# Kernel optimization log

Hardware: AMD Instinct MI355X
Metric: run time of the kernel (lower is better)

## Reference

```python
import jax, jax.numpy as jnp
import numpy as np

N = 100000      # nodes
E = 1600000     # edges (avg degree 16)
H = 128         # hidden channels
L = 5           # num_layers (only valid range 4<num_layers<8 for this module; 4 index-errors)
ALPHA = 0.1
THETA = 0.5
EPS = 1e-5      # BatchNorm1d default eps


def setup_inputs() -> dict:
    key = jax.random.key(0)
    ks = jax.random.split(key, 8)
    x = jax.random.normal(ks[0], (N, H), dtype=jnp.float32)
    W_in = jax.random.normal(ks[1], (H, H), dtype=jnp.float32) / np.float32(np.sqrt(H))
    b_in = jnp.zeros((H,), jnp.float32)
    conv_W = jax.random.normal(ks[2], (L, H, H), dtype=jnp.float32) / np.float32(np.sqrt(H))
    bn_gamma = jnp.ones((L - 1, H), jnp.float32)
    bn_beta = jnp.zeros((L - 1, H), jnp.float32)
    W_jk = jax.random.normal(ks[3], (4 * H, H), dtype=jnp.float32) / np.float32(np.sqrt(4 * H))
    b_jk = jnp.zeros((H,), jnp.float32)
    src = jax.random.randint(ks[4], (E,), 0, N, dtype=jnp.int32).astype(jnp.int64)
    dst = jax.random.randint(ks[5], (E,), 0, N, dtype=jnp.int32).astype(jnp.int64)
    return dict(x=x, W_in=W_in, b_in=b_in, conv_W=conv_W, bn_gamma=bn_gamma,
                bn_beta=bn_beta, W_jk=W_jk, b_jk=b_jk, src=src, dst=dst)


def _batchnorm(z, gamma, beta):
    # BatchNorm1d, training-mode batch statistics over the node dimension
    m = z.mean(axis=0)
    v = z.var(axis=0)
    return (z - m) * jax.lax.rsqrt(v + EPS) * gamma + beta


def reference(x, W_in, b_in, conv_W, bn_gamma, bn_beta, W_jk, b_jk, src, dst):
    # lins[0]
    z = x @ W_in + b_in          # [N, H]
    x0 = z                       # initial residual for GCNII
    zs = []
    for i in range(L):
        # GCN2Conv (shared_weights=True, normalize=False):
        #   msg = A @ z  (sparse propagation over edge list)
        msg = jax.ops.segment_sum(z[src], dst, num_segments=N)   # [N, H]
        h = (1.0 - ALPHA) * msg + ALPHA * x0
        beta_l = float(np.log(THETA / (i + 1) + 1.0))
        z = (1.0 - beta_l) * h + beta_l * (h @ conv_W[i])
        zs.append(z)
        if i % 4 == 3:
            # JumpingKnowledge('cat') over the 4 layer outputs, then lins[-1].
            # (Original code also applies BN here but immediately overwrites z,
            #  so that BN is dead computation and is skipped.)
            z = jnp.concatenate(zs[:4], axis=-1) @ W_jk + b_jk   # [N, H]
        elif i < L - 1:
            z = jax.nn.relu(_batchnorm(z, bn_gamma[i], bn_beta[i]))
    return z
```

## Files before the change

kernel.cpp:

```cpp
#include <hip/hip_runtime.h>
#include <hip/hip_bf16.h>
#include <cmath>
#include <cstddef>

#define NN 100000
#define HH 128
#define EE 1600000
#define NH (NN * HH)
#define ALPHA_C 0.1f
#define THETA_C 0.5f
#define EPS_C 1e-5f

constexpr int TR = 64;
constexpr int AST = 68;
constexpr int SCAN_B = 256;
constexpr int NBLK = (NN + SCAN_B - 1) / SCAN_B;

__global__ __launch_bounds__(256) void zero_int_k(int* __restrict__ p, int n) {
    int i = blockIdx.x * 256 + threadIdx.x;
    if (i < n) p[i] = 0;
}
__global__ __launch_bounds__(256) void zero_f4_k(float4* __restrict__ p, int n4) {
    int i = blockIdx.x * 256 + threadIdx.x;
    if (i < n4) p[i] = float4{0.f, 0.f, 0.f, 0.f};
}

__global__ void detect_idx64(const int* __restrict__ p, int* __restrict__ flag) {
    int any = 0;
    for (int i = 0; i < 64; ++i) any |= p[2 * i + 1];
    *flag = (any == 0) ? 1 : 0;
}

__device__ __forceinline__ int load_idx(const void* p, int e, int is64) {
    return is64 ? (int)((const long long*)p)[e] : ((const int*)p)[e];
}

__global__ __launch_bounds__(256) void hist_k(
    const void* __restrict__ dstp, const int* __restrict__ flag,
    int* __restrict__ hist)
{
    int e = blockIdx.x * 256 + threadIdx.x;
    if (e >= EE) return;
    atomicAdd(&hist[load_idx(dstp, e, *flag)], 1);
}

__global__ __launch_bounds__(SCAN_B) void scan1_k(
    const int* __restrict__ hist, int* __restrict__ incl, int* __restrict__ bsum)
{
    __shared__ int sh[SCAN_B];
    int t = threadIdx.x;
    int i = blockIdx.x * SCAN_B + t;
    int v = (i < NN) ? hist[i] : 0;
    sh[t] = v;
    __syncthreads();
    for (int off = 1; off < SCAN_B; off <<= 1) {
        int x = (t >= off) ? sh[t - off] : 0;
        __syncthreads();
        sh[t] += x;
        __syncthreads();
    }
    if (i < NN) incl[i] = sh[t];
    if (t == SCAN_B - 1) bsum[blockIdx.x] = sh[t];
}

__global__ __launch_bounds__(512) void scan2_k(int* __restrict__ bsum) {
    __shared__ int sh[512];
    int t = threadIdx.x;
    sh[t] = (t < NBLK) ? bsum[t] : 0;
    __syncthreads();
    for (int off = 1; off < 512; off <<= 1) {
        int x = (t >= off) ? sh[t - off] : 0;
        __syncthreads();
        sh[t] += x;
        __syncthreads();
    }
    if (t < NBLK) bsum[t] = sh[t];
}

__global__ __launch_bounds__(SCAN_B) void scan3_k(
    const int* __restrict__ hist, const int* __restrict__ incl,
    const int* __restrict__ bsum, int* __restrict__ row_ptr,
    int* __restrict__ cursor)
{
    int b = blockIdx.x;
    int i = b * SCAN_B + threadIdx.x;
    if (i < NN) {
        int ex = incl[i] - hist[i] + (b > 0 ? bsum[b - 1] : 0);
        row_ptr[i] = ex;
        cursor[i] = ex;
    }
    if (i == 0) row_ptr[NN] = EE;
}

__global__ __launch_bounds__(256) void fill_k(
    const void* __restrict__ srcp, const void* __restrict__ dstp,
    const int* __restrict__ flag, int* __restrict__ cursor,
    int* __restrict__ sorted_src)
{
    int e = blockIdx.x * 256 + threadIdx.x;
    if (e >= EE) return;
    int is64 = *flag;
    int d = load_idx(dstp, e, is64);
    int pos = atomicAdd(&cursor[d], 1);
    sorted_src[pos] = load_idx(srcp, e, is64);
}

__global__ __launch_bounds__(256) void gather_k(
    const float* __restrict__ z, const int* __restrict__ row_ptr,
    const int* __restrict__ sorted_src,
    const float* __restrict__ stats,
    const float* __restrict__ gamma, const float* __restrict__ beta,
    float* __restrict__ msg)
{
    int node = blockIdx.x * 4 + (threadIdx.x >> 6);
    if (node >= NN) return;
    int lane = threadIdx.x & 63;
    int half = lane >> 5;
    int c4 = lane & 31;

    const bool bn = (stats != nullptr);
    float4 sc = {1.f, 1.f, 1.f, 1.f}, sh = {0.f, 0.f, 0.f, 0.f};
    if (bn) {
        const float invN = 1.f / (float)NN;
        float4 s  = ((const float4*)stats)[c4];
        float4 s2 = ((const float4*)(stats + 128))[c4];
        float4 g  = ((const float4*)gamma)[c4];
        float4 b  = ((const float4*)beta)[c4];
        float m, var;
        m = s.x * invN; var = s2.x * invN - m * m;
        sc.x = rsqrtf(var + EPS_C) * g.x; sh.x = b.x - m * sc.x;
        m = s.y * invN; var = s2.y * invN - m * m;
        sc.y = rsqrtf(var + EPS_C) * g.y; sh.y = b.y - m * sc.y;
        m = s.z * invN; var = s2.z * invN - m * m;
        sc.z = rsqrtf(var + EPS_C) * g.z; sh.z = b.z - m * sc.z;
        m = s.w * invN; var = s2.w * invN - m * m;
        sc.w = rsqrtf(var + EPS_C) * g.w; sh.w = b.w - m * sc.w;
    }

    int e0 = row_ptr[node], e1 = row_ptr[node + 1];
    float4 acc = {0.f, 0.f, 0.f, 0.f};
    for (int e = e0 + half; e < e1; e += 2) {
        int s = sorted_src[e];
        float4 v = ((const float4*)(z + (size_t)s * HH))[c4];
        if (bn) {
            v.x = fmaxf(0.f, v.x * sc.x + sh.x);
            v.y = fmaxf(0.f, v.y * sc.y + sh.y);
            v.z = fmaxf(0.f, v.z * sc.z + sh.z);
            v.w = fmaxf(0.f, v.w * sc.w + sh.w);
        }
        acc.x += v.x; acc.y += v.y; acc.z += v.z; acc.w += v.w;
    }
    acc.x += __shfl_down(acc.x, 32);
    acc.y += __shfl_down(acc.y, 32);
    acc.z += __shfl_down(acc.z, 32);
    acc.w += __shfl_down(acc.w, 32);
    if (half == 0)
        ((float4*)(msg + (size_t)node * HH))[c4] = acc;
}

__global__ __launch_bounds__(256) void prep_w(
    const float* __restrict__ W_in, const float* __restrict__ conv_W,
    float* __restrict__ Wp)
{
    int i = blockIdx.y;
    int idx = blockIdx.x * 256 + threadIdx.x;
    float v;
    if (i == 0) {
        v = W_in[idx];
    } else {
        float bl = logf(THETA_C / (float)i + 1.f);
        int k = idx >> 7, c = idx & 127;
        v = bl * conv_W[(size_t)(i - 1) * 16384 + idx] + ((k == c) ? (1.f - bl) : 0.f);
    }
    Wp[(size_t)i * 16384 + idx] = v;
}

__global__ __launch_bounds__(256, 4) void gemm128(
    const float* __restrict__ src0, const float* __restrict__ src1,
    float cA, float cB, const float* __restrict__ Wp,
    const float* __restrict__ bias, float* __restrict__ out,
    float* __restrict__ statsp, int nrows)
{
    __shared__ float As[HH * AST];
    const int t = threadIdx.x;
    const int tx = t & 31;
    const int ty = t >> 5;
    const int lane = t & 63, w = t >> 6;
    const int row0 = blockIdx.x * TR;
    const bool useB = (cB != 0.f);

#pragma unroll
    for (int i = 0; i < 8; ++i) {
        int r = (i & 3) * 16 + (lane & 15);
        int k4 = ((i >> 2) * 4 + w) * 4 + (lane >> 4);
        float4 v = {0.f, 0.f, 0.f, 0.f};
        if (row0 + r < nrows) {
            float4 a = ((const float4*)(src0 + (size_t)(row0 + r) * HH))[k4];
            if (useB) {
                float4 b = ((const float4*)(src1 + (size_t)(row0 + r) * HH))[k4];
                v.x = cA * a.x + cB * b.x; v.y = cA * a.y + cB * b.y;
                v.z = cA * a.z + cB * b.z; v.w = cA * a.w + cB * b.w;
            } else {
                v.x = cA * a.x; v.y = cA * a.y; v.z = cA * a.z; v.w = cA * a.w;
            }
        }
        int k = k4 * 4;
        As[(k + 0) * AST + r] = v.x;
        As[(k + 1) * AST + r] = v.y;
        As[(k + 2) * AST + r] = v.z;
        As[(k + 3) * AST + r] = v.w;
    }
    __syncthreads();

    float acc[8][4];
#pragma unroll
    for (int ii = 0; ii < 8; ++ii)
#pragma unroll
        for (int j = 0; j < 4; ++j) acc[ii][j] = 0.f;

    const float4* W4 = (const float4*)Wp;
    float4 wbuf[4];
#pragma unroll
    for (int kk = 0; kk < 4; ++kk) wbuf[kk] = W4[kk * 32 + tx];

    for (int k0 = 0; k0 < HH; k0 += 4) {
        float4 wn[4];
        const bool more = (k0 + 4 < HH);
#pragma unroll
        for (int kk = 0; kk < 4; ++kk) {
            if (more) wn[kk] = W4[(k0 + 4 + kk) * 32 + tx];
            int k = k0 + kk;
            const float* ap = &As[k * AST + ty * 8];
            float4 a0 = *(const float4*)ap;
            float4 a1 = *(const float4*)(ap + 4);
            float a[8] = {a0.x, a0.y, a0.z, a0.w, a1.x, a1.y, a1.z, a1.w};
#pragma unroll
            for (int ii = 0; ii < 8; ++ii) {
                acc[ii][0] += a[ii] * wbuf[kk].x;
                acc[ii][1] += a[ii] * wbuf[kk].y;
                acc[ii][2] += a[ii] * wbuf[kk].z;
                acc[ii][3] += a[ii] * wbuf[kk].w;
            }
        }
        if (more) {
#pragma unroll
            for (int kk = 0; kk < 4; ++kk) wbuf[kk] = wn[kk];
        }
    }

    float4 b4 = {0.f, 0.f, 0.f, 0.f};
    if (bias) b4 = ((const float4*)bias)[tx];
    float cs[4] = {0.f, 0.f, 0.f, 0.f}, cq[4] = {0.f, 0.f, 0.f, 0.f};
    const bool doStats = (statsp != nullptr);
#pragma unroll
    for (int ii = 0; ii < 8; ++ii) {
        int r = row0 + ty * 8 + ii;
        if (r < nrows) {
            float4 v = {acc[ii][0] + b4.x, acc[ii][1] + b4.y,
                        acc[ii][2] + b4.z, acc[ii][3] + b4.w};
            ((float4*)out)[(size_t)r * 32 + tx] = v;
            if (doStats) {
                cs[0] += v.x; cq[0] += v.x * v.x;
                cs[1] += v.y; cq[1] += v.y * v.y;
                cs[2] += v.z; cq[2] += v.z * v.z;
                cs[3] += v.w; cq[3] += v.w * v.w;
            }
        }
    }
    if (doStats) {
        __syncthreads();
        float* red = As;
#pragma unroll
        for (int j = 0; j < 4; ++j) {
            red[ty * 128 + tx * 4 + j] = cs[j];
            red[1024 + ty * 128 + tx * 4 + j] = cq[j];
        }
        __syncthreads();
        if (t < 128) {
            float s = 0.f, q = 0.f;
#pragma unroll
            for (int g = 0; g < 8; ++g) {
                s += red[g * 128 + t];
                q += red[1024 + g * 128 + t];
            }
            atomicAdd(&statsp[t], s);
            atomicAdd(&statsp[128 + t], q);
        }
    }
}

__global__ __launch_bounds__(256, 4) void gemm_jk(
    const float* __restrict__ z0, const float* __restrict__ z1,
    const float* __restrict__ z2, const float* __restrict__ z3,
    const float* __restrict__ Wjk, const float* __restrict__ bjk,
    float* __restrict__ out, int nrows)
{
    __shared__ float As[HH * AST];
    const int t = threadIdx.x;
    const int tx = t & 31;
    const int ty = t >> 5;
    const int lane = t & 63, w = t >> 6;
    const int row0 = blockIdx.x * TR;

    float acc[8][4];
#pragma unroll
    for (int ii = 0; ii < 8; ++ii)
#pragma unroll
        for (int j = 0; j < 4; ++j) acc[ii][j] = 0.f;

    const float* srcs[4] = {z0, z1, z2, z3};
    for (int j = 0; j < 4; ++j) {
        if (j) __syncthreads();
        const float* Z = srcs[j];
#pragma unroll
        for (int i = 0; i < 8; ++i) {
            int r = (i & 3) * 16 + (lane & 15);
            int k4 = ((i >> 2) * 4 + w) * 4 + (lane >> 4);
            float4 v = {0.f, 0.f, 0.f, 0.f};
            if (row0 + r < nrows)
                v = ((const float4*)(Z + (size_t)(row0 + r) * HH))[k4];
            int k = k4 * 4;
            As[(k + 0) * AST + r] = v.x;
            As[(k + 1) * AST + r] = v.y;
            As[(k + 2) * AST + r] = v.z;
            As[(k + 3) * AST + r] = v.w;
        }
        __syncthreads();

        const float4* W4 = (const float4*)(Wjk + (size_t)j * 128 * HH);
        float4 wbuf[4];
#pragma unroll
        for (int kk = 0; kk < 4; ++kk) wbuf[kk] = W4[kk * 32 + tx];

        for (int k0 = 0; k0 < HH; k0 += 4) {
            float4 wn[4];
            const bool more = (k0 + 4 < HH);
#pragma unroll
            for (int kk = 0; kk < 4; ++kk) {
                if (more) wn[kk] = W4[(k0 + 4 + kk) * 32 + tx];
                int k = k0 + kk;
                const float* ap = &As[k * AST + ty * 8];
                float4 a0 = *(const float4*)ap;
                float4 a1 = *(const float4*)(ap + 4);
                float a[8] = {a0.x, a0.y, a0.z, a0.w, a1.x, a1.y, a1.z, a1.w};
#pragma unroll
                for (int ii = 0; ii < 8; ++ii) {
                    acc[ii][0] += a[ii] * wbuf[kk].x;
                    acc[ii][1] += a[ii] * wbuf[kk].y;
                    acc[ii][2] += a[ii] * wbuf[kk].z;
                    acc[ii][3] += a[ii] * wbuf[kk].w;
                }
            }
            if (more) {
#pragma unroll
                for (int kk = 0; kk < 4; ++kk) wbuf[kk] = wn[kk];
            }
        }
    }

    float4 b4 = ((const float4*)bjk)[tx];
#pragma unroll
    for (int ii = 0; ii < 8; ++ii) {
        int r = row0 + ty * 8 + ii;
        if (r < nrows) {
            float4 v = {acc[ii][0] + b4.x, acc[ii][1] + b4.y,
                        acc[ii][2] + b4.z, acc[ii][3] + b4.w};
            ((float4*)out)[(size_t)r * 32 + tx] = v;
        }
    }
}

extern "C" void kernel_launch(void* const* d_in, const int* in_sizes, int n_in,
                              void* d_out, int out_size, void* d_ws, size_t ws_size,
                              hipStream_t stream)
{
    const float* x       = (const float*)d_in[0];
    const float* W_in    = (const float*)d_in[1];
    const float* b_in    = (const float*)d_in[2];
    const float* conv_W  = (const float*)d_in[3];
    const float* bn_g    = (const float*)d_in[4];
    const float* bn_b    = (const float*)d_in[5];
    const float* W_jk    = (const float*)d_in[6];
    const float* b_jk    = (const float*)d_in[7];
    const void*  srcp    = d_in[8];
    const void*  dstp    = d_in[9];

    float* ws     = (float*)d_ws;
    float* x0     = ws;
    float* msg    = ws + (size_t)NH;
    float* zs0    = ws + 2 * (size_t)NH;
    float* zs1    = ws + 3 * (size_t)NH;
    float* zs2    = ws + 4 * (size_t)NH;
    float* stats3 = ws + 5 * (size_t)NH;
    int*   flag       = (int*)(stats3 + 768);
    int*   hist       = flag + 1;
    int*   incl       = hist + NN;
    int*   row_ptr    = incl + NN;
    int*   cursor     = row_ptr + NN + 1;
    int*   bsum       = cursor + NN;
    int*   sorted_src = bsum + NBLK + 1;
    float* Wp         = (float*)(sorted_src + EE);

    const int GEMM_GRID = (NN + TR - 1) / TR;
    const int EDGE_GRID = (EE + 255) / 256;
    const int NODE_GRID = (NN + 3) / 4;

    detect_idx64<<<1, 1, 0, stream>>>((const int*)srcp, flag);
    zero_int_k<<<(NN + 255) / 256, 256, 0, stream>>>(hist, NN);
    zero_f4_k<<<1, 192, 0, stream>>>((float4*)stats3, 192);
    hist_k<<<EDGE_GRID, 256, 0, stream>>>(dstp, flag, hist);
    scan1_k<<<NBLK, SCAN_B, 0, stream>>>(hist, incl, bsum);
    scan2_k<<<1, 512, 0, stream>>>(bsum);
    scan3_k<<<NBLK, SCAN_B, 0, stream>>>(hist, incl, bsum, row_ptr, cursor);
    fill_k<<<EDGE_GRID, 256, 0, stream>>>(srcp, dstp, flag, cursor, sorted_src);
    prep_w<<<dim3(64, 6), 256, 0, stream>>>(W_in, conv_W, Wp);

    gemm128<<<GEMM_GRID, 256, 0, stream>>>(x, x, 1.f, 0.f, Wp, b_in, x0,
                                           nullptr, NN);

    const float* act = x0;
    const float* stats_cur = nullptr;
    const float* g_cur = nullptr;
    const float* b_cur = nullptr;

    for (int i = 0; i < 5; ++i) {
        gather_k<<<NODE_GRID, 256, 0, stream>>>(act, row_ptr, sorted_src,
                                                stats_cur, g_cur, b_cur, msg);

        float* zraw = (i >= 3) ? (float*)d_out : (zs0 + (size_t)i * NH);
        float* stats_next = (i < 3) ? (stats3 + (size_t)i * 256) : nullptr;
        gemm128<<<GEMM_GRID, 256, 0, stream>>>(msg, x0, 1.f - ALPHA_C, ALPHA_C,
                                               Wp + (size_t)(i + 1) * 16384,
                                               nullptr, zraw, stats_next, NN);
        if (i < 3) {
            act = zraw;
            stats_cur = stats_next;
            g_cur = bn_g + (size_t)i * HH;
            b_cur = bn_b + (size_t)i * HH;
        } else if (i == 3) {
            gemm_jk<<<GEMM_GRID, 256, 0, stream>>>(zs0, zs1, zs2,
                                                   (const float*)d_out, W_jk, b_jk,
                                                   zs0, NN);
            act = zs0;
            stats_cur = nullptr;
            g_cur = nullptr;
            b_cur = nullptr;
        }
    }
}
```

Baseline: 1.603 ms.

## Enlarge GEMM tiles to 128x128 with 8x8 per-thread blocking and swizzled LDS; unroll gather

```diff
diff --git a/kernel.cpp b/kernel.cpp
--- a/kernel.cpp
+++ b/kernel.cpp
@@ -11,8 +11,7 @@
 #define THETA_C 0.5f
 #define EPS_C 1e-5f
 
-constexpr int TR = 64;
-constexpr int AST = 68;
+constexpr int TR = 128;
 constexpr int SCAN_B = 256;
 constexpr int NBLK = (NN + SCAN_B - 1) / SCAN_B;
 
@@ -137,9 +136,29 @@
         sc.w = rsqrtf(var + EPS_C) * g.w; sh.w = b.w - m * sc.w;
     }
 
-    int e0 = row_ptr[node], e1 = row_ptr[node + 1];
+    int e1 = row_ptr[node + 1];
+    int e = row_ptr[node] + half;
     float4 acc = {0.f, 0.f, 0.f, 0.f};
-    for (int e = e0 + half; e < e1; e += 2) {
+    float4 acc2 = {0.f, 0.f, 0.f, 0.f};
+    for (; e + 2 < e1; e += 4) {
+        int s0 = sorted_src[e];
+        int s1 = sorted_src[e + 2];
+        float4 v0 = ((const float4*)(z + (size_t)s0 * HH))[c4];
+        float4 v1 = ((const float4*)(z + (size_t)s1 * HH))[c4];
+        if (bn) {
+            v0.x = fmaxf(0.f, v0.x * sc.x + sh.x);
+            v0.y = fmaxf(0.f, v0.y * sc.y + sh.y);
+            v0.z = fmaxf(0.f, v0.z * sc.z + sh.z);
+            v0.w = fmaxf(0.f, v0.w * sc.w + sh.w);
+            v1.x = fmaxf(0.f, v1.x * sc.x + sh.x);
+            v1.y = fmaxf(0.f, v1.y * sc.y + sh.y);
+            v1.z = fmaxf(0.f, v1.z * sc.z + sh.z);
+            v1.w = fmaxf(0.f, v1.w * sc.w + sh.w);
+        }
+        acc.x += v0.x; acc.y += v0.y; acc.z += v0.z; acc.w += v0.w;
+        acc2.x += v1.x; acc2.y += v1.y; acc2.z += v1.z; acc2.w += v1.w;
+    }
+    if (e < e1) {
         int s = sorted_src[e];
         float4 v = ((const float4*)(z + (size_t)s * HH))[c4];
         if (bn) {
@@ -150,6 +169,7 @@
         }
         acc.x += v.x; acc.y += v.y; acc.z += v.z; acc.w += v.w;
     }
+    acc.x += acc2.x; acc.y += acc2.y; acc.z += acc2.z; acc.w += acc2.w;
     acc.x += __shfl_down(acc.x, 32);
     acc.y += __shfl_down(acc.y, 32);
     acc.z += __shfl_down(acc.z, 32);
@@ -175,24 +195,24 @@
     Wp[(size_t)i * 16384 + idx] = v;
 }
 
-__global__ __launch_bounds__(256, 4) void gemm128(
+__global__ __launch_bounds__(256, 2) void gemm128(
     const float* __restrict__ src0, const float* __restrict__ src1,
     float cA, float cB, const float* __restrict__ Wp,
     const float* __restrict__ bias, float* __restrict__ out,
     float* __restrict__ statsp, int nrows)
 {
-    __shared__ float As[HH * AST];
+    __shared__ float As[HH * 128];
     const int t = threadIdx.x;
-    const int tx = t & 31;
-    const int ty = t >> 5;
+    const int tx = t & 15;
+    const int ty = t >> 4;
     const int lane = t & 63, w = t >> 6;
     const int row0 = blockIdx.x * TR;
     const bool useB = (cB != 0.f);
 
 #pragma unroll
-    for (int i = 0; i < 8; ++i) {
-        int r = (i & 3) * 16 + (lane & 15);
-        int k4 = ((i >> 2) * 4 + w) * 4 + (lane >> 4);
+    for (int i = 0; i < 16; ++i) {
+        int r = (i & 7) * 16 + (lane & 15);
+        int k4 = ((i >> 3) * 4 + w) * 4 + (lane >> 4);
         float4 v = {0.f, 0.f, 0.f, 0.f};
         if (row0 + r < nrows) {
             float4 a = ((const float4*)(src0 + (size_t)(row0 + r) * HH))[k4];
@@ -205,65 +225,85 @@
             }
         }
         int k = k4 * 4;
-        As[(k + 0) * AST + r] = v.x;
-        As[(k + 1) * AST + r] = v.y;
-        As[(k + 2) * AST + r] = v.z;
-        As[(k + 3) * AST + r] = v.w;
+        int rs = r ^ ((k4 & 1) << 4);
+        As[(k + 0) * 128 + rs] = v.x;
+        As[(k + 1) * 128 + rs] = v.y;
+        As[(k + 2) * 128 + rs] = v.z;
+        As[(k + 3) * 128 + rs] = v.w;
     }
     __syncthreads();
 
-    float acc[8][4];
+    float acc[8][8];
 #pragma unroll
     for (int ii = 0; ii < 8; ++ii)
 #pragma unroll
-        for (int j = 0; j < 4; ++j) acc[ii][j] = 0.f;
+        for (int j = 0; j < 8; ++j) acc[ii][j] = 0.f;
 
     const float4* W4 = (const float4*)Wp;
-    float4 wbuf[4];
-#pragma unroll
-    for (int kk = 0; kk < 4; ++kk) wbuf[kk] = W4[kk * 32 + tx];
+    float4 wbA[4], wbB[4];
+#pragma unroll
+    for (int kk = 0; kk < 4; ++kk) {
+        wbA[kk] = W4[kk * 32 + tx];
+        wbB[kk] = W4[kk * 32 + 16 + tx];
+    }
+    const int ty8 = ty * 8;
 
     for (int k0 = 0; k0 < HH; k0 += 4) {
-        float4 wn[4];
+        float4 wnA[4], wnB[4];
         const bool more = (k0 + 4 < HH);
+        const int abase = ty8 ^ (((k0 >> 2) & 1) << 4);
 #pragma unroll
         for (int kk = 0; kk < 4; ++kk) {
-            if (more) wn[kk] = W4[(k0 + 4 + kk) * 32 + tx];
-            int k = k0 + kk;
-            const float* ap = &As[k * AST + ty * 8];
+            if (more) {
+                wnA[kk] = W4[(k0 + 4 + kk) * 32 + tx];
+                wnB[kk] = W4[(k0 + 4 + kk) * 32 + 16 + tx];
+            }
+            const float* ap = &As[(k0 + kk) * 128 + abase];
             float4 a0 = *(const float4*)ap;
             float4 a1 = *(const float4*)(ap + 4);
             float a[8] = {a0.x, a0.y, a0.z, a0.w, a1.x, a1.y, a1.z, a1.w};
+            float4 wA = wbA[kk], wB = wbB[kk];
 #pragma unroll
             for (int ii = 0; ii < 8; ++ii) {
-                acc[ii][0] += a[ii] * wbuf[kk].x;
-                acc[ii][1] += a[ii] * wbuf[kk].y;
-                acc[ii][2] += a[ii] * wbuf[kk].z;
-                acc[ii][3] += a[ii] * wbuf[kk].w;
+                acc[ii][0] += a[ii] * wA.x; acc[ii][1] += a[ii] * wA.y;
+                acc[ii][2] += a[ii] * wA.z; acc[ii][3] += a[ii] * wA.w;
+                acc[ii][4] += a[ii] * wB.x; acc[ii][5] += a[ii] * wB.y;
+                acc[ii][6] += a[ii] * wB.z; acc[ii][7] += a[ii] * wB.w;
             }
         }
         if (more) {
 #pragma unroll
-            for (int kk = 0; kk < 4; ++kk) wbuf[kk] = wn[kk];
-        }
-    }
-
-    float4 b4 = {0.f, 0.f, 0.f, 0.f};
-    if (bias) b4 = ((const float4*)bias)[tx];
-    float cs[4] = {0.f, 0.f, 0.f, 0.f}, cq[4] = {0.f, 0.f, 0.f, 0.f};
+            for (int kk = 0; kk < 4; ++kk) { wbA[kk] = wnA[kk]; wbB[kk] = wnB[kk]; }
+        }
+    }
+
+    float4 bA = {0.f, 0.f, 0.f, 0.f}, bB = {0.f, 0.f, 0.f, 0.f};
+    if (bias) {
+        bA = ((const float4*)bias)[tx];
+        bB = ((const float4*)bias)[16 + tx];
+    }
+    float cs[8] = {0.f, 0.f, 0.f, 0.f, 0.f, 0.f, 0.f, 0.f};
+    float cq[8] = {0.f, 0.f, 0.f, 0.f, 0.f, 0.f, 0.f, 0.f};
     const bool doStats = (statsp != nullptr);
 #pragma unroll
     for (int ii = 0; ii < 8; ++ii) {
-        int r = row0 + ty * 8 + ii;
+        int r = row0 + ty8 + ii;
         if (r < nrows) {
-            float4 v = {acc[ii][0] + b4.x, acc[ii][1] + b4.y,
-                        acc[ii][2] + b4.z, acc[ii][3] + b4.w};
-            ((float4*)out)[(size_t)r * 32 + tx] = v;
+            float4 vA = {acc[ii][0] + bA.x, acc[ii][1] + bA.y,
+                         acc[ii][2] + bA.z, acc[ii][3] + bA.w};
+            float4 vB = {acc[ii][4] + bB.x, acc[ii][5] + bB.y,
+                         acc[ii][6] + bB.z, acc[ii][7] + bB.w};
+            ((float4*)out)[(size_t)r * 32 + tx] = vA;
+            ((float4*)out)[(size_t)r * 32 + 16 + tx] = vB;
             if (doStats) {
-                cs[0] += v.x; cq[0] += v.x * v.x;
-                cs[1] += v.y; cq[1] += v.y * v.y;
-                cs[2] += v.z; cq[2] += v.z * v.z;
-                cs[3] += v.w; cq[3] += v.w * v.w;
+                cs[0] += vA.x; cq[0] += vA.x * vA.x;
+                cs[1] += vA.y; cq[1] += vA.y * vA.y;
+                cs[2] += vA.z; cq[2] += vA.z * vA.z;
+                cs[3] += vA.w; cq[3] += vA.w * vA.w;
+                cs[4] += vB.x; cq[4] += vB.x * vB.x;
+                cs[5] += vB.y; cq[5] += vB.y * vB.y;
+                cs[6] += vB.z; cq[6] += vB.z * vB.z;
+                cs[7] += vB.w; cq[7] += vB.w * vB.w;
             }
         }
     }
@@ -273,15 +313,17 @@
 #pragma unroll
         for (int j = 0; j < 4; ++j) {
             red[ty * 128 + tx * 4 + j] = cs[j];
-            red[1024 + ty * 128 + tx * 4 + j] = cq[j];
+            red[ty * 128 + 64 + tx * 4 + j] = cs[4 + j];
+            red[2048 + ty * 128 + tx * 4 + j] = cq[j];
+            red[2048 + ty * 128 + 64 + tx * 4 + j] = cq[4 + j];
         }
         __syncthreads();
         if (t < 128) {
             float s = 0.f, q = 0.f;
 #pragma unroll
-            for (int g = 0; g < 8; ++g) {
+            for (int g = 0; g < 16; ++g) {
                 s += red[g * 128 + t];
-                q += red[1024 + g * 128 + t];
+                q += red[2048 + g * 128 + t];
             }
             atomicAdd(&statsp[t], s);
             atomicAdd(&statsp[128 + t], q);
@@ -289,83 +331,97 @@
     }
 }
 
-__global__ __launch_bounds__(256, 4) void gemm_jk(
+__global__ __launch_bounds__(256, 2) void gemm_jk(
     const float* __restrict__ z0, const float* __restrict__ z1,
     const float* __restrict__ z2, const float* __restrict__ z3,
     const float* __restrict__ Wjk, const float* __restrict__ bjk,
     float* __restrict__ out, int nrows)
 {
-    __shared__ float As[HH * AST];
+    __shared__ float As[HH * 128];
     const int t = threadIdx.x;
-    const int tx = t & 31;
-    const int ty = t >> 5;
+    const int tx = t & 15;
+    const int ty = t >> 4;
     const int lane = t & 63, w = t >> 6;
     const int row0 = blockIdx.x * TR;
-
-    float acc[8][4];
+    const int ty8 = ty * 8;
+
+    float acc[8][8];
 #pragma unroll
     for (int ii = 0; ii < 8; ++ii)
 #pragma unroll
-        for (int j = 0; j < 4; ++j) acc[ii][j] = 0.f;
+        for (int j = 0; j < 8; ++j) acc[ii][j] = 0.f;
 
     const float* srcs[4] = {z0, z1, z2, z3};
+#pragma unroll
     for (int j = 0; j < 4; ++j) {
         if (j) __syncthreads();
         const float* Z = srcs[j];
 #pragma unroll
-        for (int i = 0; i < 8; ++i) {
-            int r = (i & 3) * 16 + (lane & 15);
-            int k4 = ((i >> 2) * 4 + w) * 4 + (lane >> 4);
+        for (int i = 0; i < 16; ++i) {
+            int r = (i & 7) * 16 + (lane & 15);
+            int k4 = ((i >> 3) * 4 + w) * 4 + (lane >> 4);
             float4 v = {0.f, 0.f, 0.f, 0.f};
             if (row0 + r < nrows)
                 v = ((const float4*)(Z + (size_t)(row0 + r) * HH))[k4];
             int k = k4 * 4;
-            As[(k + 0) * AST + r] = v.x;
-            As[(k + 1) * AST + r] = v.y;
-            As[(k + 2) * AST + r] = v.z;
-            As[(k + 3) * AST + r] = v.w;
+            int rs = r ^ ((k4 & 1) << 4);
+            As[(k + 0) * 128 + rs] = v.x;
+            As[(k + 1) * 128 + rs] = v.y;
+            As[(k + 2) * 128 + rs] = v.z;
+            As[(k + 3) * 128 + rs] = v.w;
         }
         __syncthreads();
 
         const float4* W4 = (const float4*)(Wjk + (size_t)j * 128 * HH);
-        float4 wbuf[4];
-#pragma unroll
-        for (int kk = 0; kk < 4; ++kk) wbuf[kk] = W4[kk * 32 + tx];
+        float4 wbA[4], wbB[4];
+#pragma unroll
+        for (int kk = 0; kk < 4; ++kk) {
+            wbA[kk] = W4[kk * 32 + tx];
+            wbB[kk] = W4[kk * 32 + 16 + tx];
+        }
 
         for (int k0 = 0; k0 < HH; k0 += 4) {
-            float4 wn[4];
+            float4 wnA[4], wnB[4];
             const bool more = (k0 + 4 < HH);
+            const int abase = ty8 ^ (((k0 >> 2) & 1) << 4);
 #pragma unroll
             for (int kk = 0; kk < 4; ++kk) {
-                if (more) wn[kk] = W4[(k0 + 4 + kk) * 32 + tx];
-                int k = k0 + kk;
-                const float* ap = &As[k * AST + ty * 8];
+                if (more) {
+                    wnA[kk] = W4[(k0 + 4 + kk) * 32 + tx];
+                    wnB[kk] = W4[(k0 + 4 + kk) * 32 + 16 + tx];
+                }
+                const float* ap = &As[(k0 + kk) * 128 + abase];
                 float4 a0 = *(const float4*)ap;
                 float4 a1 = *(const float4*)(ap + 4);
                 float a[8] = {a0.x, a0.y, a0.z, a0.w, a1.x, a1.y, a1.z, a1.w};
+                float4 wA = wbA[kk], wB = wbB[kk];
 #pragma unroll
                 for (int ii = 0; ii < 8; ++ii) {
-                    acc[ii][0] += a[ii] * wbuf[kk].x;
-                    acc[ii][1] += a[ii] * wbuf[kk].y;
-                    acc[ii][2] += a[ii] * wbuf[kk].z;
-                    acc[ii][3] += a[ii] * wbuf[kk].w;
+                    acc[ii][0] += a[ii] * wA.x; acc[ii][1] += a[ii] * wA.y;
+                    acc[ii][2] += a[ii] * wA.z; acc[ii][3] += a[ii] * wA.w;
+                    acc[ii][4] += a[ii] * wB.x; acc[ii][5] += a[ii] * wB.y;
+                    acc[ii][6] += a[ii] * wB.z; acc[ii][7] += a[ii] * wB.w;
                 }
             }
             if (more) {
 #pragma unroll
-                for (int kk = 0; kk < 4; ++kk) wbuf[kk] = wn[kk];
-            }
-        }
-    }
-
-    float4 b4 = ((const float4*)bjk)[tx];
+                for (int kk = 0; kk < 4; ++kk) { wbA[kk] = wnA[kk]; wbB[kk] = wnB[kk]; }
+            }
+        }
+    }
+
+    float4 bA = ((const float4*)bjk)[tx];
+    float4 bB = ((const float4*)bjk)[16 + tx];
 #pragma unroll
     for (int ii = 0; ii < 8; ++ii) {
-        int r = row0 + ty * 8 + ii;
+        int r = row0 + ty8 + ii;
         if (r < nrows) {
-            float4 v = {acc[ii][0] + b4.x, acc[ii][1] + b4.y,
-                        acc[ii][2] + b4.z, acc[ii][3] + b4.w};
-            ((float4*)out)[(size_t)r * 32 + tx] = v;
+            float4 vA = {acc[ii][0] + bA.x, acc[ii][1] + bA.y,
+                         acc[ii][2] + bA.z, acc[ii][3] + bA.w};
+            float4 vB = {acc[ii][4] + bB.x, acc[ii][5] + bB.y,
+                         acc[ii][6] + bB.z, acc[ii][7] + bB.w};
+            ((float4*)out)[(size_t)r * 32 + tx] = vA;
+            ((float4*)out)[(size_t)r * 32 + 16 + tx] = vB;
         }
     }
 }
```

New measurement: 1.680 ms. 4.8% more time.

## Fuse residual mix into gather, load GEMM A directly from global, unroll gather

Applied to the files above, without the earlier changes.

```diff
diff --git a/kernel.cpp b/kernel.cpp
--- a/kernel.cpp
+++ b/kernel.cpp
@@ -11,10 +11,11 @@
 #define THETA_C 0.5f
 #define EPS_C 1e-5f
 
-constexpr int TR = 64;
-constexpr int AST = 68;
+constexpr int TRG = 64;
 constexpr int SCAN_B = 256;
 constexpr int NBLK = (NN + SCAN_B - 1) / SCAN_B;
+
+#define AK(v, kk) ((kk) == 0 ? (v).x : (kk) == 1 ? (v).y : (kk) == 2 ? (v).z : (v).w)
 
 __global__ __launch_bounds__(256) void zero_int_k(int* __restrict__ p, int n) {
     int i = blockIdx.x * 256 + threadIdx.x;
@@ -110,6 +111,7 @@
     const int* __restrict__ sorted_src,
     const float* __restrict__ stats,
     const float* __restrict__ gamma, const float* __restrict__ beta,
+    const float* __restrict__ resid,
     float* __restrict__ msg)
 {
     int node = blockIdx.x * 4 + (threadIdx.x >> 6);
@@ -117,6 +119,8 @@
     int lane = threadIdx.x & 63;
     int half = lane >> 5;
     int c4 = lane & 31;
+
+    float4 r4 = ((const float4*)(resid + (size_t)node * HH))[c4];
 
     const bool bn = (stats != nullptr);
     float4 sc = {1.f, 1.f, 1.f, 1.f}, sh = {0.f, 0.f, 0.f, 0.f};
@@ -137,9 +141,29 @@
         sc.w = rsqrtf(var + EPS_C) * g.w; sh.w = b.w - m * sc.w;
     }
 
-    int e0 = row_ptr[node], e1 = row_ptr[node + 1];
+    int e1 = row_ptr[node + 1];
+    int e = row_ptr[node] + half;
     float4 acc = {0.f, 0.f, 0.f, 0.f};
-    for (int e = e0 + half; e < e1; e += 2) {
+    float4 acc2 = {0.f, 0.f, 0.f, 0.f};
+    for (; e + 2 < e1; e += 4) {
+        int s0 = sorted_src[e];
+        int s1 = sorted_src[e + 2];
+        float4 v0 = ((const float4*)(z + (size_t)s0 * HH))[c4];
+        float4 v1 = ((const float4*)(z + (size_t)s1 * HH))[c4];
+        if (bn) {
+            v0.x = fmaxf(0.f, v0.x * sc.x + sh.x);
+            v0.y = fmaxf(0.f, v0.y * sc.y + sh.y);
+            v0.z = fmaxf(0.f, v0.z * sc.z + sh.z);
+            v0.w = fmaxf(0.f, v0.w * sc.w + sh.w);
+            v1.x = fmaxf(0.f, v1.x * sc.x + sh.x);
+            v1.y = fmaxf(0.f, v1.y * sc.y + sh.y);
+            v1.z = fmaxf(0.f, v1.z * sc.z + sh.z);
+            v1.w = fmaxf(0.f, v1.w * sc.w + sh.w);
+        }
+        acc.x += v0.x; acc.y += v0.y; acc.z += v0.z; acc.w += v0.w;
+        acc2.x += v1.x; acc2.y += v1.y; acc2.z += v1.z; acc2.w += v1.w;
+    }
+    if (e < e1) {
         int s = sorted_src[e];
         float4 v = ((const float4*)(z + (size_t)s * HH))[c4];
         if (bn) {
@@ -150,12 +174,17 @@
         }
         acc.x += v.x; acc.y += v.y; acc.z += v.z; acc.w += v.w;
     }
+    acc.x += acc2.x; acc.y += acc2.y; acc.z += acc2.z; acc.w += acc2.w;
     acc.x += __shfl_down(acc.x, 32);
     acc.y += __shfl_down(acc.y, 32);
     acc.z += __shfl_down(acc.z, 32);
     acc.w += __shfl_down(acc.w, 32);
-    if (half == 0)
-        ((float4*)(msg + (size_t)node * HH))[c4] = acc;
+    if (half == 0) {
+        const float cA = 1.f - ALPHA_C, cB = ALPHA_C;
+        float4 o = {cA * acc.x + cB * r4.x, cA * acc.y + cB * r4.y,
+                    cA * acc.z + cB * r4.z, cA * acc.w + cB * r4.w};
+        ((float4*)(msg + (size_t)node * HH))[c4] = o;
+    }
 }
 
 __global__ __launch_bounds__(256) void prep_w(
@@ -175,42 +204,19 @@
     Wp[(size_t)i * 16384 + idx] = v;
 }
 
-__global__ __launch_bounds__(256, 4) void gemm128(
-    const float* __restrict__ src0, const float* __restrict__ src1,
-    float cA, float cB, const float* __restrict__ Wp,
+__global__ __launch_bounds__(256, 3) void gemm128(
+    const float* __restrict__ A, const float* __restrict__ Wp,
     const float* __restrict__ bias, float* __restrict__ out,
     float* __restrict__ statsp, int nrows)
 {
-    __shared__ float As[HH * AST];
+    __shared__ float red[2048];
     const int t = threadIdx.x;
     const int tx = t & 31;
     const int ty = t >> 5;
-    const int lane = t & 63, w = t >> 6;
-    const int row0 = blockIdx.x * TR;
-    const bool useB = (cB != 0.f);
-
-#pragma unroll
-    for (int i = 0; i < 8; ++i) {
-        int r = (i & 3) * 16 + (lane & 15);
-        int k4 = ((i >> 2) * 4 + w) * 4 + (lane >> 4);
-        float4 v = {0.f, 0.f, 0.f, 0.f};
-        if (row0 + r < nrows) {
-            float4 a = ((const float4*)(src0 + (size_t)(row0 + r) * HH))[k4];
-            if (useB) {
-                float4 b = ((const float4*)(src1 + (size_t)(row0 + r) * HH))[k4];
-                v.x = cA * a.x + cB * b.x; v.y = cA * a.y + cB * b.y;
-                v.z = cA * a.z + cB * b.z; v.w = cA * a.w + cB * b.w;
-            } else {
-                v.x = cA * a.x; v.y = cA * a.y; v.z = cA * a.z; v.w = cA * a.w;
-            }
-        }
-        int k = k4 * 4;
-        As[(k + 0) * AST + r] = v.x;
-        As[(k + 1) * AST + r] = v.y;
-        As[(k + 2) * AST + r] = v.z;
-        As[(k + 3) * AST + r] = v.w;
-    }
-    __syncthreads();
+    const int row0o = blockIdx.x * TRG;
+    const int row0 = (row0o <= nrows - TRG) ? row0o : (nrows - TRG);
+    const float4* Ab = (const float4*)(A + (size_t)(row0 + ty * 8) * HH);
+    const float4* W4 = (const float4*)Wp;
 
     float acc[8][4];
 #pragma unroll
@@ -218,33 +224,37 @@
 #pragma unroll
         for (int j = 0; j < 4; ++j) acc[ii][j] = 0.f;
 
-    const float4* W4 = (const float4*)Wp;
-    float4 wbuf[4];
-#pragma unroll
-    for (int kk = 0; kk < 4; ++kk) wbuf[kk] = W4[kk * 32 + tx];
+    float4 ac[8], wc[4];
+#pragma unroll
+    for (int ii = 0; ii < 8; ++ii) ac[ii] = Ab[ii * 32];
+#pragma unroll
+    for (int kk = 0; kk < 4; ++kk) wc[kk] = W4[kk * 32 + tx];
 
     for (int k0 = 0; k0 < HH; k0 += 4) {
-        float4 wn[4];
         const bool more = (k0 + 4 < HH);
+        const int c4n = (k0 >> 2) + 1;
+        float4 an[8], wn[4];
+        if (more) {
+#pragma unroll
+            for (int kk = 0; kk < 4; ++kk) wn[kk] = W4[(k0 + 4 + kk) * 32 + tx];
+#pragma unroll
+            for (int ii = 0; ii < 8; ++ii) an[ii] = Ab[ii * 32 + c4n];
+        }
 #pragma unroll
         for (int kk = 0; kk < 4; ++kk) {
-            if (more) wn[kk] = W4[(k0 + 4 + kk) * 32 + tx];
-            int k = k0 + kk;
-            const float* ap = &As[k * AST + ty * 8];
-            float4 a0 = *(const float4*)ap;
-            float4 a1 = *(const float4*)(ap + 4);
-            float a[8] = {a0.x, a0.y, a0.z, a0.w, a1.x, a1.y, a1.z, a1.w};
+            float4 w = wc[kk];
 #pragma unroll
             for (int ii = 0; ii < 8; ++ii) {
-                acc[ii][0] += a[ii] * wbuf[kk].x;
-                acc[ii][1] += a[ii] * wbuf[kk].y;
-                acc[ii][2] += a[ii] * wbuf[kk].z;
-                acc[ii][3] += a[ii] * wbuf[kk].w;
+                float a = AK(ac[ii], kk);
+                acc[ii][0] += a * w.x; acc[ii][1] += a * w.y;
+                acc[ii][2] += a * w.z; acc[ii][3] += a * w.w;
             }
         }
         if (more) {
 #pragma unroll
-            for (int kk = 0; kk < 4; ++kk) wbuf[kk] = wn[kk];
+            for (int ii = 0; ii < 8; ++ii) ac[ii] = an[ii];
+#pragma unroll
+            for (int kk = 0; kk < 4; ++kk) wc[kk] = wn[kk];
         }
     }
 
@@ -255,7 +265,7 @@
 #pragma unroll
     for (int ii = 0; ii < 8; ++ii) {
         int r = row0 + ty * 8 + ii;
-        if (r < nrows) {
+        if (r >= row0o) {
             float4 v = {acc[ii][0] + b4.x, acc[ii][1] + b4.y,
                         acc[ii][2] + b4.z, acc[ii][3] + b4.w};
             ((float4*)out)[(size_t)r * 32 + tx] = v;
@@ -268,8 +278,6 @@
         }
     }
     if (doStats) {
-        __syncthreads();
-        float* red = As;
 #pragma unroll
         for (int j = 0; j < 4; ++j) {
             red[ty * 128 + tx * 4 + j] = cs[j];
@@ -289,18 +297,18 @@
     }
 }
 
-__global__ __launch_bounds__(256, 4) void gemm_jk(
+__global__ __launch_bounds__(256, 3) void gemm_jk(
     const float* __restrict__ z0, const float* __restrict__ z1,
     const float* __restrict__ z2, const float* __restrict__ z3,
     const float* __restrict__ Wjk, const float* __restrict__ bjk,
-    float* __restrict__ out, int nrows)
-{
-    __shared__ float As[HH * AST];
+    float* out, int nrows)
+{
     const int t = threadIdx.x;
     const int tx = t & 31;
     const int ty = t >> 5;
-    const int lane = t & 63, w = t >> 6;
-    const int row0 = blockIdx.x * TR;
+    const int row0o = blockIdx.x * TRG;
+    const int row0 = (row0o <= nrows - TRG) ? row0o : (nrows - TRG);
+    const size_t roff = (size_t)(row0 + ty * 8) * HH;
 
     float acc[8][4];
 #pragma unroll
@@ -309,51 +317,42 @@
         for (int j = 0; j < 4; ++j) acc[ii][j] = 0.f;
 
     const float* srcs[4] = {z0, z1, z2, z3};
+#pragma unroll
     for (int j = 0; j < 4; ++j) {
-        if (j) __syncthreads();
-        const float* Z = srcs[j];
-#pragma unroll
-        for (int i = 0; i < 8; ++i) {
-            int r = (i & 3) * 16 + (lane & 15);
-            int k4 = ((i >> 2) * 4 + w) * 4 + (lane >> 4);
-            float4 v = {0.f, 0.f, 0.f, 0.f};
-            if (row0 + r < nrows)
-                v = ((const float4*)(Z + (size_t)(row0 + r) * HH))[k4];
-            int k = k4 * 4;
-            As[(k + 0) * AST + r] = v.x;
-            As[(k + 1) * AST + r] = v.y;
-            As[(k + 2) * AST + r] = v.z;
-            As[(k + 3) * AST + r] = v.w;
-        }
-        __syncthreads();
-
+        const float4* Ab = (const float4*)(srcs[j] + roff);
         const float4* W4 = (const float4*)(Wjk + (size_t)j * 128 * HH);
-        float4 wbuf[4];
-#pragma unroll
-        for (int kk = 0; kk < 4; ++kk) wbuf[kk] = W4[kk * 32 + tx];
+
+        float4 ac[8], wc[4];
+#pragma unroll
+        for (int ii = 0; ii < 8; ++ii) ac[ii] = Ab[ii * 32];
+#pragma unroll
+        for (int kk = 0; kk < 4; ++kk) wc[kk] = W4[kk * 32 + tx];
 
         for (int k0 = 0; k0 < HH; k0 += 4) {
-            float4 wn[4];
             const bool more = (k0 + 4 < HH);
+            const int c4n = (k0 >> 2) + 1;
+            float4 an[8], wn[4];
+            if (more) {
+#pragma unroll
+                for (int kk = 0; kk < 4; ++kk) wn[kk] = W4[(k0 + 4 + kk) * 32 + tx];
+#pragma unroll
+                for (int ii = 0; ii < 8; ++ii) an[ii] = Ab[ii * 32 + c4n];
+            }
 #pragma unroll
             for (int kk = 0; kk < 4; ++kk) {
-                if (more) wn[kk] = W4[(k0 + 4 + kk) * 32 + tx];
-                int k = k0 + kk;
-                const float* ap = &As[k * AST + ty * 8];
-                float4 a0 = *(const float4*)ap;
-                float4 a1 = *(const float4*)(ap + 4);
-                float a[8] = {a0.x, a0.y, a0.z, a0.w, a1.x, a1.y, a1.z, a1.w};
+                float4 w = wc[kk];
 #pragma unroll
                 for (int ii = 0; ii < 8; ++ii) {
-                    acc[ii][0] += a[ii] * wbuf[kk].x;
-                    acc[ii][1] += a[ii] * wbuf[kk].y;
-                    acc[ii][2] += a[ii] * wbuf[kk].z;
-                    acc[ii][3] += a[ii] * wbuf[kk].w;
+                    float a = AK(ac[ii], kk);
+                    acc[ii][0] += a * w.x; acc[ii][1] += a * w.y;
+                    acc[ii][2] += a * w.z; acc[ii][3] += a * w.w;
                 }
             }
             if (more) {
 #pragma unroll
-                for (int kk = 0; kk < 4; ++kk) wbuf[kk] = wn[kk];
+                for (int ii = 0; ii < 8; ++ii) ac[ii] = an[ii];
+#pragma unroll
+                for (int kk = 0; kk < 4; ++kk) wc[kk] = wn[kk];
             }
         }
     }
@@ -362,7 +361,7 @@
 #pragma unroll
     for (int ii = 0; ii < 8; ++ii) {
         int r = row0 + ty * 8 + ii;
-        if (r < nrows) {
+        if (r >= row0o) {
             float4 v = {acc[ii][0] + b4.x, acc[ii][1] + b4.y,
                         acc[ii][2] + b4.z, acc[ii][3] + b4.w};
             ((float4*)out)[(size_t)r * 32 + tx] = v;
@@ -401,7 +400,7 @@
     int*   sorted_src = bsum + NBLK + 1;
     float* Wp         = (float*)(sorted_src + EE);
 
-    const int GEMM_GRID = (NN + TR - 1) / TR;
+    const int GEMM_GRID = (NN + TRG - 1) / TRG;
     const int EDGE_GRID = (EE + 255) / 256;
     const int NODE_GRID = (NN + 3) / 4;
 
@@ -415,8 +414,7 @@
     fill_k<<<EDGE_GRID, 256, 0, stream>>>(srcp, dstp, flag, cursor, sorted_src);
     prep_w<<<dim3(64, 6), 256, 0, stream>>>(W_in, conv_W, Wp);
 
-    gemm128<<<GEMM_GRID, 256, 0, stream>>>(x, x, 1.f, 0.f, Wp, b_in, x0,
-                                           nullptr, NN);
+    gemm128<<<GEMM_GRID, 256, 0, stream>>>(x, Wp, b_in, x0, nullptr, NN);
 
     const float* act = x0;
     const float* stats_cur = nullptr;
@@ -425,12 +423,11 @@
 
     for (int i = 0; i < 5; ++i) {
         gather_k<<<NODE_GRID, 256, 0, stream>>>(act, row_ptr, sorted_src,
-                                                stats_cur, g_cur, b_cur, msg);
+                                                stats_cur, g_cur, b_cur, x0, msg);
 
         float* zraw = (i >= 3) ? (float*)d_out : (zs0 + (size_t)i * NH);
         float* stats_next = (i < 3) ? (stats3 + (size_t)i * 256) : nullptr;
-        gemm128<<<GEMM_GRID, 256, 0, stream>>>(msg, x0, 1.f - ALPHA_C, ALPHA_C,
-                                               Wp + (size_t)(i + 1) * 16384,
+        gemm128<<<GEMM_GRID, 256, 0, stream>>>(msg, Wp + (size_t)(i + 1) * 16384,
                                                nullptr, zraw, stats_next, NN);
         if (i < 3) {
             act = zraw;
```

New measurement: 1.762 ms. 9.9% more time.
